# Performance work log

Hardware: AMD Instinct MI355X
Metric: run time of the kernel (lower is better)

## Reference

```python
import jax, jax.numpy as jnp
import numpy as np

N = 50000      # nodes
E = 400000     # edges (before self loops)
G = 8          # graphs in the batch
H = 128        # latent width (message_passer out_channels)
F_IN = 5       # raw node features
F_MASK = 3     # mask features (last col = BC indicator)
F_EDGE = 3     # edge_feature_dim
OUT = 3        # x-vel, y-vel, pressure
REPEATS = 3    # message passing rounds


def _mlp2(x, W1, b1, W2, b2):
    return jax.nn.relu(x @ W1 + b1) @ W2 + b2


def _seg_mean(v, ids, num):
    s = jax.ops.segment_sum(v, ids, num_segments=num)
    c = jax.ops.segment_sum(jnp.ones((v.shape[0],), v.dtype), ids, num_segments=num)
    return s / jnp.maximum(c, 1.0)[:, None]


def setup_inputs() -> dict:
    key = jax.random.key(0)
    ks = jax.random.split(key, 16)
    x = jax.random.normal(ks[0], (N, F_IN), jnp.float32)
    x_mask = (jax.random.uniform(ks[1], (N, F_MASK)) < 0.2).astype(jnp.float32)
    edge_index = jax.random.randint(ks[2], (2, E), 0, N, dtype=jnp.int32)
    edge_attr = jax.random.normal(ks[3], (E, F_EDGE), jnp.float32)
    pos = jax.random.uniform(ks[4], (N, 2), dtype=jnp.float32)
    batch = jnp.sort(jax.random.randint(ks[5], (N,), 0, G, dtype=jnp.int32))
    lin = lambda k, i, o: jax.random.normal(k, (i, o), jnp.float32) * (1.0 / np.sqrt(i))
    return {
        'x': x, 'x_mask': x_mask, 'edge_attr': edge_attr, 'pos': pos,
        'W_e1': lin(ks[6], F_IN + F_MASK, H), 'b_e1': jnp.zeros((H,), jnp.float32),
        'W_e2': lin(ks[7], H, H), 'b_e2': jnp.zeros((H,), jnp.float32),
        'W_m1': lin(ks[8], 2 * H + F_EDGE, H), 'b_m1': jnp.zeros((H,), jnp.float32),
        'W_m2': lin(ks[9], H, H), 'b_m2': jnp.zeros((H,), jnp.float32),
        'W_u1': lin(ks[10], 4 * H, H), 'b_u1': jnp.zeros((H,), jnp.float32),
        'W_u2': lin(ks[11], H, H), 'b_u2': jnp.zeros((H,), jnp.float32),
        'W_d1': lin(ks[12], H, H), 'b_d1': jnp.zeros((H,), jnp.float32),
        'W_d2': lin(ks[13], H, OUT), 'b_d2': jnp.zeros((OUT,), jnp.float32),
        'edge_index': edge_index, 'batch': batch,
    }


def reference(x, x_mask, edge_attr, pos,
              W_e1, b_e1, W_e2, b_e2,
              W_m1, b_m1, W_m2, b_m2,
              W_u1, b_u1, W_u2, b_u2,
              W_d1, b_d1, W_d2, b_d2,
              edge_index, batch):
    n = x.shape[0]
    bc = x_mask[:, -1]                                   # BC indicator (0/1)
    h = jnp.concatenate([x, x_mask], axis=1)             # [N, F_IN+F_MASK]
    # add self loops with zero edge attributes
    sl = jnp.arange(n, dtype=edge_index.dtype)
    ei = jnp.concatenate([edge_index, jnp.stack([sl, sl])], axis=1)
    ea = jnp.concatenate([edge_attr, jnp.zeros((n, edge_attr.shape[1]), edge_attr.dtype)], axis=0)
    # encoder
    h = _mlp2(h, W_e1, b_e1, W_e2, b_e2)                 # [N, H]
    # BC scatter-mean per graph and global mean pool
    bc_cnt = jax.ops.segment_sum(bc, batch, num_segments=G)
    x_BC = jax.ops.segment_sum(h * bc[:, None], batch, num_segments=G) / jnp.maximum(bc_cnt, 1.0)[:, None]
    x_graph = _seg_mean(h, batch, G)
    src, dst = ei[0], ei[1]
    for _ in range(REPEATS):
        m = _mlp2(jnp.concatenate([h[src], h[dst], ea], axis=1), W_m1, b_m1, W_m2, b_m2)
        agg = _seg_mean(m, dst, n)                       # mean aggregation at dst
        upd_in = jnp.concatenate([h, agg, x_graph[batch], x_BC[batch]], axis=1)
        h = h + _mlp2(upd_in, W_u1, b_u1, W_u2, b_u2)
        x_graph = _seg_mean(h, batch, G)
    return _mlp2(h, W_d1, b_d1, W_d2, b_d2)              # [N, OUT]
```

## Files before the change

kernel.cpp:

```cpp
#include <hip/hip_runtime.h>


#define NN 50000
#define EE 400000
#define GG 8
#define NBLK 196
#define SGRID 512

typedef __attribute__((ext_vector_type(8))) short short8;
typedef __attribute__((ext_vector_type(4))) float floatx4;

__device__ __forceinline__ unsigned short f2bf(float x) {
    unsigned u = __float_as_uint(x);
    u += 0x7FFF + ((u >> 16) & 1);
    return (unsigned short)(u >> 16);
}
__device__ __forceinline__ float bf2f(unsigned short h) {
    return __uint_as_float(((unsigned)h) << 16);
}
__device__ __forceinline__ void cvt8(const float* v, short8& hi, short8& lo) {
#pragma unroll
    for (int j = 0; j < 8; ++j) {
        unsigned short h = f2bf(v[j]);
        hi[j] = (short)h;
        lo[j] = (short)f2bf(v[j] - bf2f(h));
    }
}

__global__ void k_count(const int* __restrict__ ei, int* __restrict__ deg) {
    int i = blockIdx.x * 256 + threadIdx.x;
    if (i < EE) atomicAdd(&deg[ei[EE + i]], 1);
}

__global__ __launch_bounds__(256) void k_scan1(const int* __restrict__ deg, int* __restrict__ ex,
                                               int* __restrict__ blksum) {
    __shared__ int s[256];
    const int t = threadIdx.x;
    int i = blockIdx.x * 256 + t;
    int v = (i < NN) ? deg[i] : 0;
    s[t] = v;
    __syncthreads();
    for (int off = 1; off < 256; off <<= 1) {
        int x = (t >= off) ? s[t - off] : 0;
        __syncthreads();
        s[t] += x;
        __syncthreads();
    }
    if (i < NN) ex[i] = s[t] - v;
    if (t == 255) blksum[blockIdx.x] = s[255];
}

__global__ __launch_bounds__(256) void k_scan2(int* __restrict__ blksum) {
    __shared__ int s[256];
    const int t = threadIdx.x;
    int v = (t < NBLK) ? blksum[t] : 0;
    s[t] = v;
    __syncthreads();
    for (int off = 1; off < 256; off <<= 1) {
        int x = (t >= off) ? s[t - off] : 0;
        __syncthreads();
        s[t] += x;
        __syncthreads();
    }
    if (t < NBLK) blksum[t] = s[t] - v;
}

__global__ void k_scan3(const int* __restrict__ ex, const int* __restrict__ blkoff,
                        int* __restrict__ row_ptr, int* __restrict__ cursor) {
    int i = blockIdx.x * 256 + threadIdx.x;
    if (i < NN) {
        int v = ex[i] + blkoff[blockIdx.x];
        row_ptr[i] = v;
        cursor[i] = v;
    }
    if (i == 0) row_ptr[NN] = EE;
}

__global__ void k_scatter(const int* __restrict__ ei, const float* __restrict__ ea,
                          int* __restrict__ cursor, int* __restrict__ src_sorted,
                          float4* __restrict__ ea_s) {
    int e = blockIdx.x * 256 + threadIdx.x;
    if (e >= EE) return;
    int s = ei[e], d = ei[EE + e];
    int p = atomicAdd(&cursor[d], 1);
    src_sorted[p] = s;
    ea_s[p] = make_float4(ea[3 * e], ea[3 * e + 1], ea[3 * e + 2], 0.f);
}

__global__ __launch_bounds__(256) void k_counts(const int* __restrict__ batch, const float* __restrict__ xm,
                                                float* __restrict__ cnt_node, float* __restrict__ cnt_bc) {
    __shared__ float cn[8], cb[8];
    const int t = threadIdx.x;
    if (t < 8) { cn[t] = 0.f; cb[t] = 0.f; }
    __syncthreads();
    int i = blockIdx.x * 256 + t;
    if (i < NN) {
        int g = batch[i];
        atomicAdd(&cn[g], 1.f);
        atomicAdd(&cb[g], xm[3 * i + 2]);
    }
    __syncthreads();
    if (t < 8) {
        if (cn[t] != 0.f) atomicAdd(&cnt_node[t], cn[t]);
        if (cb[t] != 0.f) atomicAdd(&cnt_bc[t], cb[t]);
    }
}

__global__ __launch_bounds__(256) void k_wfuse(const float* __restrict__ Wm2, const float* __restrict__ Wu1,
                                               float* __restrict__ Wf) {
    int idx = blockIdx.x * 256 + threadIdx.x;
    int r = idx >> 7, c = idx & 127;
    float s = 0.f;
    for (int k = 0; k < 128; ++k) s += Wm2[r * 128 + k] * Wu1[(128 + k) * 128 + c];
    Wf[idx] = s;
}
__global__ void k_bfuse(const float* __restrict__ bm2, const float* __restrict__ Wu1,
                        const float* __restrict__ bu1, float* __restrict__ bf) {
    int c = threadIdx.x;
    float s = bu1[c];
    for (int k = 0; k < 128; ++k) s += bm2[k] * Wu1[(128 + k) * 128 + c];
    bf[c] = s;
}

__global__ __launch_bounds__(256) void k_pack_all(
    const float* __restrict__ We2, const float* __restrict__ Wm1,
    const float* __restrict__ Wu1, const float* __restrict__ Wf,
    const float* __restrict__ Wu2, const float* __restrict__ Wd1,
    short* __restrict__ We2h, short* __restrict__ We2l,
    short* __restrict__ Wm1sh, short* __restrict__ Wm1sl,
    short* __restrict__ Wm1dh, short* __restrict__ Wm1dl,
    short* __restrict__ Wu1ah, short* __restrict__ Wu1al,
    short* __restrict__ Wfh, short* __restrict__ Wfl,
    short* __restrict__ Wu2h, short* __restrict__ Wu2l,
    short* __restrict__ Wd1h, short* __restrict__ Wd1l) {
    int b = blockIdx.x;
    int id = b >> 6;
    int p = (b & 63) * 256 + threadIdx.x;
    const float* W;
    short *hi, *lo;
    switch (id) {
        case 0: W = We2; hi = We2h; lo = We2l; break;
        case 1: W = Wm1; hi = Wm1sh; lo = Wm1sl; break;
        case 2: W = Wm1 + 16384; hi = Wm1dh; lo = Wm1dl; break;
        case 3: W = Wu1; hi = Wu1ah; lo = Wu1al; break;
        case 4: W = Wf; hi = Wfh; lo = Wfl; break;
        case 5: W = Wu2; hi = Wu2h; lo = Wu2l; break;
        default: W = Wd1; hi = Wd1h; lo = Wd1l; break;
    }
    int j = p & 7;
    int lane = (p >> 3) & 63;
    int chunk = p >> 9;
    int k0 = chunk & 3, nt = chunk >> 2;
    int quad = lane >> 4;
    int n = nt * 16 + (lane & 15);
    bool perm = (id == 1) || (id == 2) || (id == 5) || (id == 6);
    int k;
    if (perm) k = k0 * 32 + ((j >> 2) << 4) + (quad << 2) + (j & 3);
    else k = k0 * 32 + quad * 8 + j;
    float w = W[k * 128 + n];
    unsigned short h = f2bf(w);
    hi[p] = (short)h;
    lo[p] = (short)f2bf(w - bf2f(h));
}

__global__ __launch_bounds__(256, 2) void k_genc(
    const float* __restrict__ x, const float* __restrict__ xm,
    const float* __restrict__ We1, const float* __restrict__ be1,
    const short* __restrict__ W2h, const short* __restrict__ W2l,
    const float* __restrict__ be2,
    const short* __restrict__ Wsh, const short* __restrict__ Wsl,
    const short* __restrict__ Wdh, const short* __restrict__ Wdl,
    const float* __restrict__ bm1, const int* __restrict__ batch,
    float* __restrict__ hout, float* __restrict__ Ps, float* __restrict__ Pd,
    float* __restrict__ part_h, float* __restrict__ part_hbc) {
    __shared__ __align__(16) short sWh[16384];
    __shared__ __align__(16) short sWl[16384];
    __shared__ __align__(16) float swe[1024];
    __shared__ float sbe[128];
    __shared__ float ldsH[1024];
    __shared__ float ldsB[1024];
    const int tid = threadIdx.x;
    const int wave = tid >> 6, lane = tid & 63;
    const int m16 = lane & 15, quad = lane >> 4;
    const int t0 = blockIdx.x * 4 + wave;
    const int t1 = t0 + SGRID * 4;
    const bool h1 = (t1 < 3125);
    const int r0 = t0 * 16 + m16;
    const int r1 = (h1 ? t1 * 16 : 0) + m16;

    auto copyW = [&](const short* gh, const short* gl) {
        const float4* sH = (const float4*)gh;
        const float4* sL = (const float4*)gl;
        float4* dH = (float4*)sWh;
        float4* dL = (float4*)sWl;
#pragma unroll
        for (int u = 0; u < 8; ++u) {
            int i = tid + u * 256;
            dH[i] = sH[i];
            dL[i] = sL[i];
        }
    };

    {
        copyW(W2h, W2l);
        for (int i = tid; i < 1024; i += 256) {
            swe[i] = We1[i];
            ldsH[i] = 0.f;
            ldsB[i] = 0.f;
        }
        if (tid < 128) sbe[tid] = be1[tid];
    }
    float in0[8], in1[8];
#pragma unroll
    for (int k = 0; k < 5; ++k) { in0[k] = x[r0 * 5 + k]; in1[k] = x[r1 * 5 + k]; }
#pragma unroll
    for (int k = 0; k < 3; ++k) { in0[5 + k] = xm[r0 * 3 + k]; in1[5 + k] = xm[r1 * 3 + k]; }
    int g0 = batch[r0], g1 = batch[r1];
    __syncthreads();
    short8 ah0[4], al0[4], ah1[4], al1[4];
#pragma unroll
    for (int k0 = 0; k0 < 4; ++k0) {
        float tv[8];
#pragma unroll
        for (int j = 0; j < 8; ++j) {
            int c = k0 * 32 + quad * 8 + j;
            float s = sbe[c];
#pragma unroll
            for (int kk = 0; kk < 8; ++kk) s += in0[kk] * swe[kk * 128 + c];
            tv[j] = fmaxf(s, 0.f);
        }
        cvt8(tv, ah0[k0], al0[k0]);
    }
#pragma unroll
    for (int k0 = 0; k0 < 4; ++k0) {
        float tv[8];
#pragma unroll
        for (int j = 0; j < 8; ++j) {
            int c = k0 * 32 + quad * 8 + j;
            float s = sbe[c];
#pragma unroll
            for (int kk = 0; kk < 8; ++kk) s += in1[kk] * swe[kk * 128 + c];
            tv[j] = fmaxf(s, 0.f);
        }
        cvt8(tv, ah1[k0], al1[k0]);
    }
    const int fb = lane << 3;
    floatx4 acc0[8], acc1[8];
    auto mmacc = [&](const short8 xh0[4], const short8 xl0[4],
                     const short8 xh1[4], const short8 xl1[4]) {
#pragma unroll
        for (int k0 = 0; k0 < 4; ++k0) {
#pragma unroll
            for (int nt = 0; nt < 8; ++nt) {
                const int base = (((nt << 2) | k0) << 9) + fb;
                short8 bh = *(const short8*)&sWh[base];
                short8 bl = *(const short8*)&sWl[base];
                acc0[nt] = __builtin_amdgcn_mfma_f32_16x16x32_bf16(bh, xh0[k0], acc0[nt], 0, 0, 0);
                acc0[nt] = __builtin_amdgcn_mfma_f32_16x16x32_bf16(bl, xh0[k0], acc0[nt], 0, 0, 0);
                acc0[nt] = __builtin_amdgcn_mfma_f32_16x16x32_bf16(bh, xl0[k0], acc0[nt], 0, 0, 0);
                if (h1) {
                    acc1[nt] = __builtin_amdgcn_mfma_f32_16x16x32_bf16(bh, xh1[k0], acc1[nt], 0, 0, 0);
                    acc1[nt] = __builtin_amdgcn_mfma_f32_16x16x32_bf16(bl, xh1[k0], acc1[nt], 0, 0, 0);
                    acc1[nt] = __builtin_amdgcn_mfma_f32_16x16x32_bf16(bh, xl1[k0], acc1[nt], 0, 0, 0);
                }
            }
        }
    };

#pragma unroll
    for (int nt = 0; nt < 8; ++nt) {
        float4 bv = *(const float4*)(be2 + nt * 16 + quad * 4);
        acc0[nt][0] = bv.x; acc0[nt][1] = bv.y; acc0[nt][2] = bv.z; acc0[nt][3] = bv.w;
        acc1[nt][0] = bv.x; acc1[nt][1] = bv.y; acc1[nt][2] = bv.z; acc1[nt][3] = bv.w;
    }
    mmacc(ah0, al0, ah1, al1);
    {
        float* d0 = hout + (size_t)r0 * 128 + quad * 4;
#pragma unroll
        for (int nt = 0; nt < 8; ++nt)
            *(float4*)(d0 + nt * 16) = make_float4(acc0[nt][0], acc0[nt][1], acc0[nt][2], acc0[nt][3]);
    }
    if (h1) {
        float* d1 = hout + (size_t)r1 * 128 + quad * 4;
#pragma unroll
        for (int nt = 0; nt < 8; ++nt)
            *(float4*)(d1 + nt * 16) = make_float4(acc1[nt][0], acc1[nt][1], acc1[nt][2], acc1[nt][3]);
    }
    {
        float bc = in0[7];
        int glo = __shfl(g0, 0), ghi = __shfl(g0, 15);
        if (glo == ghi) {
#pragma unroll
            for (int nt = 0; nt < 8; ++nt) {
                float4 v = make_float4(acc0[nt][0], acc0[nt][1], acc0[nt][2], acc0[nt][3]);
                float4 w = make_float4(v.x * bc, v.y * bc, v.z * bc, v.w * bc);
#pragma unroll
                for (int off = 1; off < 16; off <<= 1) {
                    v.x += __shfl_xor(v.x, off); v.y += __shfl_xor(v.y, off);
                    v.z += __shfl_xor(v.z, off); v.w += __shfl_xor(v.w, off);
                    w.x += __shfl_xor(w.x, off); w.y += __shfl_xor(w.y, off);
                    w.z += __shfl_xor(w.z, off); w.w += __shfl_xor(w.w, off);
                }
                if (m16 == 0) {
                    float* sp = &ldsH[glo * 128 + nt * 16 + quad * 4];
                    atomicAdd(sp + 0, v.x); atomicAdd(sp + 1, v.y);
                    atomicAdd(sp + 2, v.z); atomicAdd(sp + 3, v.w);
                    float* sq = &ldsB[glo * 128 + nt * 16 + quad * 4];
                    atomicAdd(sq + 0, w.x); atomicAdd(sq + 1, w.y);
                    atomicAdd(sq + 2, w.z); atomicAdd(sq + 3, w.w);
                }
            }
        } else {
#pragma unroll
            for (int nt = 0; nt < 8; ++nt)
#pragma unroll
                for (int i = 0; i < 4; ++i) {
                    atomicAdd(&ldsH[g0 * 128 + nt * 16 + quad * 4 + i], acc0[nt][i]);
                    atomicAdd(&ldsB[g0 * 128 + nt * 16 + quad * 4 + i], acc0[nt][i] * bc);
                }
        }
    }
    if (h1) {
        float bc = in1[7];
        int glo = __shfl(g1, 0), ghi = __shfl(g1, 15);
        if (glo == ghi) {
#pragma unroll
            for (int nt = 0; nt < 8; ++nt) {
                float4 v = make_float4(acc1[nt][0], acc1[nt][1], acc1[nt][2], acc1[nt][3]);
                float4 w = make_float4(v.x * bc, v.y * bc, v.z * bc, v.w * bc);
#pragma unroll
                for (int off = 1; off < 16; off <<= 1) {
                    v.x += __shfl_xor(v.x, off); v.y += __shfl_xor(v.y, off);
                    v.z += __shfl_xor(v.z, off); v.w += __shfl_xor(v.w, off);
                    w.x += __shfl_xor(w.x, off); w.y += __shfl_xor(w.y, off);
                    w.z += __shfl_xor(w.z, off); w.w += __shfl_xor(w.w, off);
                }
                if (m16 == 0) {
                    float* sp = &ldsH[glo * 128 + nt * 16 + quad * 4];
                    atomicAdd(sp + 0, v.x); atomicAdd(sp + 1, v.y);
                    atomicAdd(sp + 2, v.z); atomicAdd(sp + 3, v.w);
                    float* sq = &ldsB[glo * 128 + nt * 16 + quad * 4];
                    atomicAdd(sq + 0, w.x); atomicAdd(sq + 1, w.y);
                    atomicAdd(sq + 2, w.z); atomicAdd(sq + 3, w.w);
                }
            }
        } else {
#pragma unroll
            for (int nt = 0; nt < 8; ++nt)
#pragma unroll
                for (int i = 0; i < 4; ++i) {
                    atomicAdd(&ldsH[g1 * 128 + nt * 16 + quad * 4 + i], acc1[nt][i]);
                    atomicAdd(&ldsB[g1 * 128 + nt * 16 + quad * 4 + i], acc1[nt][i] * bc);
                }
        }
    }
    short8 ph0[4], pl0[4], ph1[4], pl1[4];
#pragma unroll
    for (int k0 = 0; k0 < 4; ++k0) {
        float v[8] = {acc0[2 * k0][0], acc0[2 * k0][1], acc0[2 * k0][2], acc0[2 * k0][3],
                      acc0[2 * k0 + 1][0], acc0[2 * k0 + 1][1], acc0[2 * k0 + 1][2], acc0[2 * k0 + 1][3]};
        cvt8(v, ph0[k0], pl0[k0]);
    }
#pragma unroll
    for (int k0 = 0; k0 < 4; ++k0) {
        float v[8] = {acc1[2 * k0][0], acc1[2 * k0][1], acc1[2 * k0][2], acc1[2 * k0][3],
                      acc1[2 * k0 + 1][0], acc1[2 * k0 + 1][1], acc1[2 * k0 + 1][2], acc1[2 * k0 + 1][3]};
        cvt8(v, ph1[k0], pl1[k0]);
    }
    __syncthreads();
    {
        float* ph = part_h + (size_t)blockIdx.x * 1024;
        float* pb = part_hbc + (size_t)blockIdx.x * 1024;
        for (int i = tid; i < 1024; i += 256) { ph[i] = ldsH[i]; pb[i] = ldsB[i]; }
    }
    copyW(Wsh, Wsl);
    __syncthreads();
#pragma unroll
    for (int nt = 0; nt < 8; ++nt) { acc0[nt] = (floatx4)0.f; acc1[nt] = (floatx4)0.f; }
    mmacc(ph0, pl0, ph1, pl1);
    {
        float* d0 = Ps + (size_t)r0 * 128 + quad * 4;
#pragma unroll
        for (int nt = 0; nt < 8; ++nt)
            *(float4*)(d0 + nt * 16) = make_float4(acc0[nt][0], acc0[nt][1], acc0[nt][2], acc0[nt][3]);
        if (h1) {
            float* d1 = Ps + (size_t)r1 * 128 + quad * 4;
#pragma unroll
            for (int nt = 0; nt < 8; ++nt)
                *(float4*)(d1 + nt * 16) = make_float4(acc1[nt][0], acc1[nt][1], acc1[nt][2], acc1[nt][3]);
        }
    }
    __syncthreads();
    copyW(Wdh, Wdl);
    __syncthreads();
#pragma unroll
    for (int nt = 0; nt < 8; ++nt) {
        float4 bv = *(const float4*)(bm1 + nt * 16 + quad * 4);
        acc0[nt][0] = bv.x; acc0[nt][1] = bv.y; acc0[nt][2] = bv.z; acc0[nt][3] = bv.w;
        acc1[nt][0] = bv.x; acc1[nt][1] = bv.y; acc1[nt][2] = bv.z; acc1[nt][3] = bv.w;
    }
    mmacc(ph0, pl0, ph1, pl1);
    {
        float* d0 = Pd + (size_t)r0 * 128 + quad * 4;
#pragma unroll
        for (int nt = 0; nt < 8; ++nt)
            *(float4*)(d0 + nt * 16) = make_float4(acc0[nt][0], acc0[nt][1], acc0[nt][2], acc0[nt][3]);
        if (h1) {
            float* d1 = Pd + (size_t)r1 * 128 + quad * 4;
#pragma unroll
            for (int nt = 0; nt < 8; ++nt)
                *(float4*)(d1 + nt * 16) = make_float4(acc1[nt][0], acc1[nt][1], acc1[nt][2], acc1[nt][3]);
        }
    }
}

__global__ __launch_bounds__(128) void k_redstats(const float* __restrict__ part_h,
                                                  const float* __restrict__ part_hbc,
                                                  float* __restrict__ sum_h, float* __restrict__ sum_hbc) {
    const int g = blockIdx.x, c = threadIdx.x;
    float s = 0.f, sb = 0.f;
    for (int b = 0; b < SGRID; ++b) {
        s += part_h[b * 1024 + g * 128 + c];
        sb += part_hbc[b * 1024 + g * 128 + c];
    }
    sum_h[g * 128 + c] = s;
    sum_hbc[g * 128 + c] = sb;
}

template <int MODE>
__global__ __launch_bounds__(256, 2) void k_fused3(
    const float* __restrict__ hbuf, const float* __restrict__ accm,
    const short* __restrict__ W1h, const short* __restrict__ W1l,
    const short* __restrict__ W2h, const short* __restrict__ W2l,
    const short* __restrict__ W3h, const short* __restrict__ W3l,
    const short* __restrict__ Wsh, const short* __restrict__ Wsl,
    const short* __restrict__ Wdh, const short* __restrict__ Wdl,
    const float* __restrict__ gt, const float* __restrict__ bf3,
    const float* __restrict__ bu2, const float* __restrict__ bm1,
    const float* __restrict__ bd1, const float* __restrict__ Wd2,
    const float* __restrict__ bd2, const int* __restrict__ batch,
    float* __restrict__ hout, float* __restrict__ Ps, float* __restrict__ Pd,
    float* __restrict__ partf, float* __restrict__ outp) {
    __shared__ __align__(16) short sWh[16384];
    __shared__ __align__(16) short sWl[16384];
    __shared__ float ldsH[1024];
    const int tid = threadIdx.x;
    const int wave = tid >> 6, lane = tid & 63;
    const int m16 = lane & 15, quad = lane >> 4;
    const int t0 = blockIdx.x * 4 + wave;
    const int t1 = t0 + SGRID * 4;
    const bool h1 = (t1 < 3125);
    const int r0 = t0 * 16 + m16;
    const int r1 = (h1 ? t1 * 16 : 0) + m16;

    auto copyW = [&](const short* gh, const short* gl) {
        const float4* sH = (const float4*)gh;
        const float4* sL = (const float4*)gl;
        float4* dH = (float4*)sWh;
        float4* dL = (float4*)sWl;
#pragma unroll
        for (int u = 0; u < 8; ++u) {
            int i = tid + u * 256;
            dH[i] = sH[i];
            dL[i] = sL[i];
        }
    };

    const float* Ap0 = hbuf + (size_t)r0 * 128 + quad * 8;
    const float* Ap1 = hbuf + (size_t)r1 * 128 + quad * 8;
    float4 a0[8], a1[8];
#pragma unroll
    for (int k0 = 0; k0 < 4; ++k0) {
        a0[k0 * 2 + 0] = *(const float4*)(Ap0 + k0 * 32);
        a0[k0 * 2 + 1] = *(const float4*)(Ap0 + k0 * 32 + 4);
        a1[k0 * 2 + 0] = *(const float4*)(Ap1 + k0 * 32);
        a1[k0 * 2 + 1] = *(const float4*)(Ap1 + k0 * 32 + 4);
    }
    int g0 = batch[r0], g1 = batch[r1];
    if (MODE == 0) {
        for (int i = tid; i < 1024; i += 256) ldsH[i] = 0.f;
    }
    copyW(W1h, W1l);
    __syncthreads();

    short8 hh0[4], hl0[4], hh1[4], hl1[4];
#pragma unroll
    for (int k0 = 0; k0 < 4; ++k0) {
        float v[8] = {a0[k0 * 2].x, a0[k0 * 2].y, a0[k0 * 2].z, a0[k0 * 2].w,
                      a0[k0 * 2 + 1].x, a0[k0 * 2 + 1].y, a0[k0 * 2 + 1].z, a0[k0 * 2 + 1].w};
        cvt8(v, hh0[k0], hl0[k0]);
    }
#pragma unroll
    for (int k0 = 0; k0 < 4; ++k0) {
        float v[8] = {a1[k0 * 2].x, a1[k0 * 2].y, a1[k0 * 2].z, a1[k0 * 2].w,
                      a1[k0 * 2 + 1].x, a1[k0 * 2 + 1].y, a1[k0 * 2 + 1].z, a1[k0 * 2 + 1].w};
        cvt8(v, hh1[k0], hl1[k0]);
    }

    const int fb = lane << 3;
    floatx4 acc0[8], acc1[8];
    auto mmacc = [&](const short8 xh0[4], const short8 xl0[4],
                     const short8 xh1[4], const short8 xl1[4]) {
#pragma unroll
        for (int k0 = 0; k0 < 4; ++k0) {
#pragma unroll
            for (int nt = 0; nt < 8; ++nt) {
                const int base = (((nt << 2) | k0) << 9) + fb;
                short8 bh = *(const short8*)&sWh[base];
                short8 bl = *(const short8*)&sWl[base];
                acc0[nt] = __builtin_amdgcn_mfma_f32_16x16x32_bf16(bh, xh0[k0], acc0[nt], 0, 0, 0);
                acc0[nt] = __builtin_amdgcn_mfma_f32_16x16x32_bf16(bl, xh0[k0], acc0[nt], 0, 0, 0);
                acc0[nt] = __builtin_amdgcn_mfma_f32_16x16x32_bf16(bh, xl0[k0], acc0[nt], 0, 0, 0);
                if (h1) {
                    acc1[nt] = __builtin_amdgcn_mfma_f32_16x16x32_bf16(bh, xh1[k0], acc1[nt], 0, 0, 0);
                    acc1[nt] = __builtin_amdgcn_mfma_f32_16x16x32_bf16(bl, xh1[k0], acc1[nt], 0, 0, 0);
                    acc1[nt] = __builtin_amdgcn_mfma_f32_16x16x32_bf16(bh, xl1[k0], acc1[nt], 0, 0, 0);
                }
            }
        }
    };

    {
        const float* gp0 = gt + g0 * 128 + quad * 4;
        const float* gp1 = gt + g1 * 128 + quad * 4;
#pragma unroll
        for (int nt = 0; nt < 8; ++nt) {
            float4 bv = *(const float4*)(bf3 + nt * 16 + quad * 4);
            float4 gv0 = *(const float4*)(gp0 + nt * 16);
            float4 gv1 = *(const float4*)(gp1 + nt * 16);
            acc0[nt][0] = bv.x + gv0.x; acc0[nt][1] = bv.y + gv0.y;
            acc0[nt][2] = bv.z + gv0.z; acc0[nt][3] = bv.w + gv0.w;
            acc1[nt][0] = bv.x + gv1.x; acc1[nt][1] = bv.y + gv1.y;
            acc1[nt][2] = bv.z + gv1.z; acc1[nt][3] = bv.w + gv1.w;
        }
    }
    mmacc(hh0, hl0, hh1, hl1);

    const float* Cp0 = accm + (size_t)r0 * 128 + quad * 8;
    const float* Cp1 = accm + (size_t)r1 * 128 + quad * 8;
    float4 c0[8], c1[8];
#pragma unroll
    for (int k0 = 0; k0 < 4; ++k0) {
        c0[k0 * 2 + 0] = *(const float4*)(Cp0 + k0 * 32);
        c0[k0 * 2 + 1] = *(const float4*)(Cp0 + k0 * 32 + 4);
        c1[k0 * 2 + 0] = *(const float4*)(Cp1 + k0 * 32);
        c1[k0 * 2 + 1] = *(const float4*)(Cp1 + k0 * 32 + 4);
    }
    __syncthreads();
    copyW(W2h, W2l);
    __syncthreads();

    short8 ch0[4], cl0[4], ch1[4], cl1[4];
#pragma unroll
    for (int k0 = 0; k0 < 4; ++k0) {
        float v[8] = {c0[k0 * 2].x, c0[k0 * 2].y, c0[k0 * 2].z, c0[k0 * 2].w,
                      c0[k0 * 2 + 1].x, c0[k0 * 2 + 1].y, c0[k0 * 2 + 1].z, c0[k0 * 2 + 1].w};
        cvt8(v, ch0[k0], cl0[k0]);
    }
#pragma unroll
    for (int k0 = 0; k0 < 4; ++k0) {
        float v[8] = {c1[k0 * 2].x, c1[k0 * 2].y, c1[k0 * 2].z, c1[k0 * 2].w,
                      c1[k0 * 2 + 1].x, c1[k0 * 2 + 1].y, c1[k0 * 2 + 1].z, c1[k0 * 2 + 1].w};
        cvt8(v, ch1[k0], cl1[k0]);
    }
    mmacc(ch0, cl0, ch1, cl1);

    short8 ph0[4], pl0[4], ph1[4], pl1[4];
#pragma unroll
    for (int k0 = 0; k0 < 4; ++k0) {
        float v[8] = {fmaxf(acc0[2 * k0][0], 0.f), fmaxf(acc0[2 * k0][1], 0.f),
                      fmaxf(acc0[2 * k0][2], 0.f), fmaxf(acc0[2 * k0][3], 0.f),
                      fmaxf(acc0[2 * k0 + 1][0], 0.f), fmaxf(acc0[2 * k0 + 1][1], 0.f),
                      fmaxf(acc0[2 * k0 + 1][2], 0.f), fmaxf(acc0[2 * k0 + 1][3], 0.f)};
        cvt8(v, ph0[k0], pl0[k0]);
    }
#pragma unroll
    for (int k0 = 0; k0 < 4; ++k0) {
        float v[8] = {fmaxf(acc1[2 * k0][0], 0.f), fmaxf(acc1[2 * k0][1], 0.f),
                      fmaxf(acc1[2 * k0][2], 0.f), fmaxf(acc1[2 * k0][3], 0.f),
                      fmaxf(acc1[2 * k0 + 1][0], 0.f), fmaxf(acc1[2 * k0 + 1][1], 0.f),
                      fmaxf(acc1[2 * k0 + 1][2], 0.f), fmaxf(acc1[2 * k0 + 1][3], 0.f)};
        cvt8(v, ph1[k0], pl1[k0]);
    }

    {
        const float* Ep0 = hbuf + (size_t)r0 * 128 + quad * 4;
        const float* Ep1 = hbuf + (size_t)r1 * 128 + quad * 4;
#pragma unroll
        for (int nt = 0; nt < 8; ++nt) {
            float4 bv = *(const float4*)(bu2 + nt * 16 + quad * 4);
            float4 e0 = *(const float4*)(Ep0 + nt * 16);
            float4 e1 = *(const float4*)(Ep1 + nt * 16);
            acc0[nt][0] = e0.x + bv.x; acc0[nt][1] = e0.y + bv.y;
            acc0[nt][2] = e0.z + bv.z; acc0[nt][3] = e0.w + bv.w;
            acc1[nt][0] = e1.x + bv.x; acc1[nt][1] = e1.y + bv.y;
            acc1[nt][2] = e1.z + bv.z; acc1[nt][3] = e1.w + bv.w;
        }
    }
    __syncthreads();
    copyW(W3h, W3l);
    __syncthreads();
    mmacc(ph0, pl0, ph1, pl1);

    if (MODE == 0) {
        {
            float* d0 = hout + (size_t)r0 * 128 + quad * 4;
#pragma unroll
            for (int nt = 0; nt < 8; ++nt)
                *(float4*)(d0 + nt * 16) = make_float4(acc0[nt][0], acc0[nt][1], acc0[nt][2], acc0[nt][3]);
        }
        if (h1) {
            float* d1 = hout + (size_t)r1 * 128 + quad * 4;
#pragma unroll
            for (int nt = 0; nt < 8; ++nt)
                *(float4*)(d1 + nt * 16) = make_float4(acc1[nt][0], acc1[nt][1], acc1[nt][2], acc1[nt][3]);
        }
        {
            int glo = __shfl(g0, 0), ghi = __shfl(g0, 15);
            if (glo == ghi) {
#pragma unroll
                for (int nt = 0; nt < 8; ++nt) {
                    float4 v = make_float4(acc0[nt][0], acc0[nt][1], acc0[nt][2], acc0[nt][3]);
#pragma unroll
                    for (int off = 1; off < 16; off <<= 1) {
                        v.x += __shfl_xor(v.x, off);
                        v.y += __shfl_xor(v.y, off);
                        v.z += __shfl_xor(v.z, off);
                        v.w += __shfl_xor(v.w, off);
                    }
                    if (m16 == 0) {
                        float* sp = &ldsH[glo * 128 + nt * 16 + quad * 4];
                        atomicAdd(sp + 0, v.x); atomicAdd(sp + 1, v.y);
                        atomicAdd(sp + 2, v.z); atomicAdd(sp + 3, v.w);
                    }
                }
            } else {
#pragma unroll
                for (int nt = 0; nt < 8; ++nt)
#pragma unroll
                    for (int i = 0; i < 4; ++i)
                        atomicAdd(&ldsH[g0 * 128 + nt * 16 + quad * 4 + i], acc0[nt][i]);
            }
        }
        if (h1) {
            int glo = __shfl(g1, 0), ghi = __shfl(g1, 15);
            if (glo == ghi) {
#pragma unroll
                for (int nt = 0; nt < 8; ++nt) {
                    float4 v = make_float4(acc1[nt][0], acc1[nt][1], acc1[nt][2], acc1[nt][3]);
#pragma unroll
                    for (int off = 1; off < 16; off <<= 1) {
                        v.x += __shfl_xor(v.x, off);
                        v.y += __shfl_xor(v.y, off);
                        v.z += __shfl_xor(v.z, off);
                        v.w += __shfl_xor(v.w, off);
                    }
                    if (m16 == 0) {
                        float* sp = &ldsH[glo * 128 + nt * 16 + quad * 4];
                        atomicAdd(sp + 0, v.x); atomicAdd(sp + 1, v.y);
                        atomicAdd(sp + 2, v.z); atomicAdd(sp + 3, v.w);
                    }
                }
            } else {
#pragma unroll
                for (int nt = 0; nt < 8; ++nt)
#pragma unroll
                    for (int i = 0; i < 4; ++i)
                        atomicAdd(&ldsH[g1 * 128 + nt * 16 + quad * 4 + i], acc1[nt][i]);
            }
        }
#pragma unroll
        for (int k0 = 0; k0 < 4; ++k0) {
            float v[8] = {acc0[2 * k0][0], acc0[2 * k0][1], acc0[2 * k0][2], acc0[2 * k0][3],
                          acc0[2 * k0 + 1][0], acc0[2 * k0 + 1][1], acc0[2 * k0 + 1][2], acc0[2 * k0 + 1][3]};
            cvt8(v, ph0[k0], pl0[k0]);
        }
#pragma unroll
        for (int k0 = 0; k0 < 4; ++k0) {
            float v[8] = {acc1[2 * k0][0], acc1[2 * k0][1], acc1[2 * k0][2], acc1[2 * k0][3],
                          acc1[2 * k0 + 1][0], acc1[2 * k0 + 1][1], acc1[2 * k0 + 1][2], acc1[2 * k0 + 1][3]};
            cvt8(v, ph1[k0], pl1[k0]);
        }
        __syncthreads();
        {
            float* pf = partf + (size_t)blockIdx.x * 1024;
            for (int i = tid; i < 1024; i += 256) pf[i] = ldsH[i];
        }
        copyW(Wsh, Wsl);
        __syncthreads();
#pragma unroll
        for (int nt = 0; nt < 8; ++nt) { acc0[nt] = (floatx4)0.f; acc1[nt] = (floatx4)0.f; }
        mmacc(ph0, pl0, ph1, pl1);
        {
            float* d0 = Ps + (size_t)r0 * 128 + quad * 4;
#pragma unroll
            for (int nt = 0; nt < 8; ++nt)
                *(float4*)(d0 + nt * 16) = make_float4(acc0[nt][0], acc0[nt][1], acc0[nt][2], acc0[nt][3]);
            if (h1) {
                float* d1 = Ps + (size_t)r1 * 128 + quad * 4;
#pragma unroll
                for (int nt = 0; nt < 8; ++nt)
                    *(float4*)(d1 + nt * 16) = make_float4(acc1[nt][0], acc1[nt][1], acc1[nt][2], acc1[nt][3]);
            }
        }
        __syncthreads();
        copyW(Wdh, Wdl);
        __syncthreads();
#pragma unroll
        for (int nt = 0; nt < 8; ++nt) {
            float4 bv = *(const float4*)(bm1 + nt * 16 + quad * 4);
            acc0[nt][0] = bv.x; acc0[nt][1] = bv.y; acc0[nt][2] = bv.z; acc0[nt][3] = bv.w;
            acc1[nt][0] = bv.x; acc1[nt][1] = bv.y; acc1[nt][2] = bv.z; acc1[nt][3] = bv.w;
        }
        mmacc(ph0, pl0, ph1, pl1);
        {
            float* d0 = Pd + (size_t)r0 * 128 + quad * 4;
#pragma unroll
            for (int nt = 0; nt < 8; ++nt)
                *(float4*)(d0 + nt * 16) = make_float4(acc0[nt][0], acc0[nt][1], acc0[nt][2], acc0[nt][3]);
            if (h1) {
                float* d1 = Pd + (size_t)r1 * 128 + quad * 4;
#pragma unroll
                for (int nt = 0; nt < 8; ++nt)
                    *(float4*)(d1 + nt * 16) = make_float4(acc1[nt][0], acc1[nt][1], acc1[nt][2], acc1[nt][3]);
            }
        }
    } else {
#pragma unroll
        for (int k0 = 0; k0 < 4; ++k0) {
            float v[8] = {acc0[2 * k0][0], acc0[2 * k0][1], acc0[2 * k0][2], acc0[2 * k0][3],
                          acc0[2 * k0 + 1][0], acc0[2 * k0 + 1][1], acc0[2 * k0 + 1][2], acc0[2 * k0 + 1][3]};
            cvt8(v, ph0[k0], pl0[k0]);
        }
#pragma unroll
        for (int k0 = 0; k0 < 4; ++k0) {
            float v[8] = {acc1[2 * k0][0], acc1[2 * k0][1], acc1[2 * k0][2], acc1[2 * k0][3],
                          acc1[2 * k0 + 1][0], acc1[2 * k0 + 1][1], acc1[2 * k0 + 1][2], acc1[2 * k0 + 1][3]};
            cvt8(v, ph1[k0], pl1[k0]);
        }
        __syncthreads();
        copyW(Wdh, Wdl);
        __syncthreads();
#pragma unroll
        for (int nt = 0; nt < 8; ++nt) {
            float4 bv = *(const float4*)(bd1 + nt * 16 + quad * 4);
            acc0[nt][0] = bv.x; acc0[nt][1] = bv.y; acc0[nt][2] = bv.z; acc0[nt][3] = bv.w;
            acc1[nt][0] = bv.x; acc1[nt][1] = bv.y; acc1[nt][2] = bv.z; acc1[nt][3] = bv.w;
        }
        mmacc(ph0, pl0, ph1, pl1);
        float p00 = 0.f, p01 = 0.f, p02 = 0.f, p10 = 0.f, p11 = 0.f, p12 = 0.f;
#pragma unroll
        for (int nt = 0; nt < 8; ++nt) {
#pragma unroll
            for (int i = 0; i < 4; ++i) {
                int c = nt * 16 + quad * 4 + i;
                const float* wp = &Wd2[c * 3];
                float v0 = fmaxf(acc0[nt][i], 0.f);
                float v1 = fmaxf(acc1[nt][i], 0.f);
                p00 += v0 * wp[0]; p01 += v0 * wp[1]; p02 += v0 * wp[2];
                p10 += v1 * wp[0]; p11 += v1 * wp[1]; p12 += v1 * wp[2];
            }
        }
        p00 += __shfl_xor(p00, 16); p00 += __shfl_xor(p00, 32);
        p01 += __shfl_xor(p01, 16); p01 += __shfl_xor(p01, 32);
        p02 += __shfl_xor(p02, 16); p02 += __shfl_xor(p02, 32);
        p10 += __shfl_xor(p10, 16); p10 += __shfl_xor(p10, 32);
        p11 += __shfl_xor(p11, 16); p11 += __shfl_xor(p11, 32);
        p12 += __shfl_xor(p12, 16); p12 += __shfl_xor(p12, 32);
        if (quad == 0) {
            outp[r0 * 3 + 0] = p00 + bd2[0];
            outp[r0 * 3 + 1] = p01 + bd2[1];
            outp[r0 * 3 + 2] = p02 + bd2[2];
            if (h1) {
                outp[r1 * 3 + 0] = p10 + bd2[0];
                outp[r1 * 3 + 1] = p11 + bd2[1];
                outp[r1 * 3 + 2] = p12 + bd2[2];
            }
        }
    }
}

__global__ __launch_bounds__(256) void k_edge_agg(const float* __restrict__ Ps, const float* __restrict__ Pd,
                                                  const int* __restrict__ row_ptr, const int* __restrict__ src_sorted,
                                                  const float4* __restrict__ ea_s, const float* __restrict__ Wm1,
                                                  float* __restrict__ accm) {
    const int lane = threadIdx.x & 63;
    const int d = blockIdx.x * 4 + (threadIdx.x >> 6);
    const int c = lane * 2;
    const float2 w0 = *(const float2*)&Wm1[256 * 128 + c];
    const float2 w1 = *(const float2*)&Wm1[257 * 128 + c];
    const float2 w2 = *(const float2*)&Wm1[258 * 128 + c];
    const float2 pd = *(const float2*)&Pd[(size_t)d * 128 + c];
    const int beg = row_ptr[d], end = row_ptr[d + 1];
    const float2 sv = *(const float2*)&Ps[(size_t)d * 128 + c];
    float ax = fmaxf(sv.x + pd.x, 0.f);
    float ay = fmaxf(sv.y + pd.y, 0.f);
    int k = beg;
    for (; k + 3 < end; k += 4) {
        int s0 = src_sorted[k], s1 = src_sorted[k + 1], s2 = src_sorted[k + 2], s3 = src_sorted[k + 3];
        float4 e0 = ea_s[k], e1 = ea_s[k + 1], e2 = ea_s[k + 2], e3 = ea_s[k + 3];
        float2 pa = *(const float2*)&Ps[(size_t)s0 * 128 + c];
        float2 pb = *(const float2*)&Ps[(size_t)s1 * 128 + c];
        float2 pc = *(const float2*)&Ps[(size_t)s2 * 128 + c];
        float2 pe = *(const float2*)&Ps[(size_t)s3 * 128 + c];
        ax += fmaxf(pa.x + pd.x + e0.x * w0.x + e0.y * w1.x + e0.z * w2.x, 0.f)
            + fmaxf(pb.x + pd.x + e1.x * w0.x + e1.y * w1.x + e1.z * w2.x, 0.f)
            + fmaxf(pc.x + pd.x + e2.x * w0.x + e2.y * w1.x + e2.z * w2.x, 0.f)
            + fmaxf(pe.x + pd.x + e3.x * w0.x + e3.y * w1.x + e3.z * w2.x, 0.f);
        ay += fmaxf(pa.y + pd.y + e0.x * w0.y + e0.y * w1.y + e0.z * w2.y, 0.f)
            + fmaxf(pb.y + pd.y + e1.x * w0.y + e1.y * w1.y + e1.z * w2.y, 0.f)
            + fmaxf(pc.y + pd.y + e2.x * w0.y + e2.y * w1.y + e2.z * w2.y, 0.f)
            + fmaxf(pe.y + pd.y + e3.x * w0.y + e3.y * w1.y + e3.z * w2.y, 0.f);
    }
    for (; k < end; ++k) {
        int s0 = src_sorted[k];
        float4 e0 = ea_s[k];
        float2 pa = *(const float2*)&Ps[(size_t)s0 * 128 + c];
        ax += fmaxf(pa.x + pd.x + e0.x * w0.x + e0.y * w1.x + e0.z * w2.x, 0.f);
        ay += fmaxf(pa.y + pd.y + e0.x * w0.y + e0.y * w1.y + e0.z * w2.y, 0.f);
    }
    float inv = 1.f / (float)(end - beg + 1);
    *(float2*)&accm[(size_t)d * 128 + c] = make_float2(ax * inv, ay * inv);
}

template <bool PART>
__global__ __launch_bounds__(128) void k_gterm(const float* __restrict__ sum_h, const float* __restrict__ sum_hbc,
                                               const float* __restrict__ partf,
                                               const float* __restrict__ cnt_node, const float* __restrict__ cnt_bc,
                                               const float* __restrict__ Wu1, float* __restrict__ gt) {
    const int g = blockIdx.x;
    const int c = threadIdx.x;
    __shared__ float sg[128], sb[128];
    const float invn = 1.f / fmaxf(cnt_node[g], 1.f);
    const float invb = 1.f / fmaxf(cnt_bc[g], 1.f);
    float s0;
    if (PART) {
        s0 = 0.f;
        for (int b = 0; b < SGRID; ++b) s0 += partf[b * 1024 + g * 128 + c];
    } else {
        s0 = sum_h[g * 128 + c];
    }
    sg[c] = s0 * invn;
    sb[c] = sum_hbc[g * 128 + c] * invb;
    __syncthreads();
    float s = 0.f;
    for (int k = 0; k < 128; ++k) s += sg[k] * Wu1[(256 + k) * 128 + c];
    for (int k = 0; k < 128; ++k) s += sb[k] * Wu1[(384 + k) * 128 + c];
    gt[g * 128 + c] = s;
}

extern "C" void kernel_launch(void* const* d_in, const int* in_sizes, int n_in,
                              void* d_out, int out_size, void* d_ws, size_t ws_size,
                              hipStream_t stream) {
    const float* x = (const float*)d_in[0];
    const float* x_mask = (const float*)d_in[1];
    const float* edge_attr = (const float*)d_in[2];
    const float* W_e1 = (const float*)d_in[4];
    const float* b_e1 = (const float*)d_in[5];
    const float* W_e2 = (const float*)d_in[6];
    const float* b_e2 = (const float*)d_in[7];
    const float* W_m1 = (const float*)d_in[8];
    const float* b_m1 = (const float*)d_in[9];
    const float* W_m2 = (const float*)d_in[10];
    const float* b_m2 = (const float*)d_in[11];
    const float* W_u1 = (const float*)d_in[12];
    const float* b_u1 = (const float*)d_in[13];
    const float* W_u2 = (const float*)d_in[14];
    const float* b_u2 = (const float*)d_in[15];
    const float* W_d1 = (const float*)d_in[16];
    const float* b_d1 = (const float*)d_in[17];
    const float* W_d2 = (const float*)d_in[18];
    const float* b_d2 = (const float*)d_in[19];
    const int* edge_index = (const int*)d_in[20];
    const int* batch = (const int*)d_in[21];
    float* out = (float*)d_out;

    char* wp = (char*)d_ws;
    auto carve = [&](size_t bytes) {
        char* r = wp;
        wp += (bytes + 255) & ~(size_t)255;
        return r;
    };
    float* h = (float*)carve(sizeof(float) * (size_t)NN * 128);
    float* Ps = (float*)carve(sizeof(float) * (size_t)NN * 128);
    float* Pd = (float*)carve(sizeof(float) * (size_t)NN * 128);
    float* accm = (float*)carve(sizeof(float) * (size_t)NN * 128);
    float4* ea_s = (float4*)carve(sizeof(float4) * (size_t)EE);
    float* stats = (float*)carve(sizeof(float) * 4096);
    float* sum_h = stats;
    float* sum_hbc = stats + 1024;
    float* cnt_node = stats + 2048;
    float* cnt_bc = stats + 2056;
    float* gterm = stats + 2304;
    float* bfused = stats + 3328;
    float* part_h = (float*)carve(sizeof(float) * (size_t)SGRID * 1024);
    float* part_hbc = (float*)carve(sizeof(float) * (size_t)SGRID * 1024);
    float* partf = (float*)carve(sizeof(float) * (size_t)SGRID * 1024);
    int* deg = (int*)carve(sizeof(int) * NN);
    int* row_ptr = (int*)carve(sizeof(int) * (NN + 1));
    int* cursor = (int*)carve(sizeof(int) * NN);
    int* src_sorted = (int*)carve(sizeof(int) * EE);
    int* exbuf = (int*)carve(sizeof(int) * NN);
    int* blksum = (int*)carve(sizeof(int) * 256);
    float* Wf = (float*)carve(sizeof(float) * 16384);
    short* We2h = (short*)carve(sizeof(short) * 16384);
    short* We2l = (short*)carve(sizeof(short) * 16384);
    short* Wm1sh = (short*)carve(sizeof(short) * 16384);
    short* Wm1sl = (short*)carve(sizeof(short) * 16384);
    short* Wm1dh = (short*)carve(sizeof(short) * 16384);
    short* Wm1dl = (short*)carve(sizeof(short) * 16384);
    short* Wu1ah = (short*)carve(sizeof(short) * 16384);
    short* Wu1al = (short*)carve(sizeof(short) * 16384);
    short* Wfh = (short*)carve(sizeof(short) * 16384);
    short* Wfl = (short*)carve(sizeof(short) * 16384);
    short* Wu2h = (short*)carve(sizeof(short) * 16384);
    short* Wu2l = (short*)carve(sizeof(short) * 16384);
    short* Wd1h = (short*)carve(sizeof(short) * 16384);
    short* Wd1l = (short*)carve(sizeof(short) * 16384);

    const dim3 b256(256);
    const int gE256 = (EE + 255) / 256;

    hipMemsetAsync(deg, 0, sizeof(int) * NN, stream);
    hipMemsetAsync(stats, 0, sizeof(float) * 2064, stream);
    k_wfuse<<<64, b256, 0, stream>>>(W_m2, W_u1, Wf);
    k_bfuse<<<1, 128, 0, stream>>>(b_m2, W_u1, b_u1, bfused);
    k_pack_all<<<448, b256, 0, stream>>>(W_e2, W_m1, W_u1, Wf, W_u2, W_d1,
                                         We2h, We2l, Wm1sh, Wm1sl, Wm1dh, Wm1dl,
                                         Wu1ah, Wu1al, Wfh, Wfl, Wu2h, Wu2l, Wd1h, Wd1l);
    k_count<<<gE256, b256, 0, stream>>>(edge_index, deg);
    k_scan1<<<NBLK, b256, 0, stream>>>(deg, exbuf, blksum);
    k_scan2<<<1, b256, 0, stream>>>(blksum);
    k_scan3<<<NBLK, b256, 0, stream>>>(exbuf, blksum, row_ptr, cursor);
    k_scatter<<<gE256, b256, 0, stream>>>(edge_index, edge_attr, cursor, src_sorted, ea_s);
    k_counts<<<NBLK, b256, 0, stream>>>(batch, x_mask, cnt_node, cnt_bc);
    k_genc<<<SGRID, b256, 0, stream>>>(x, x_mask, W_e1, b_e1, We2h, We2l, b_e2,
                                       Wm1sh, Wm1sl, Wm1dh, Wm1dl, b_m1, batch,
                                       h, Ps, Pd, part_h, part_hbc);
    k_redstats<<<GG, 128, 0, stream>>>(part_h, part_hbc, sum_h, sum_hbc);

    for (int rep = 0; rep < 3; ++rep) {
        if (rep == 0)
            k_gterm<false><<<GG, 128, 0, stream>>>(sum_h, sum_hbc, nullptr, cnt_node, cnt_bc, W_u1, gterm);
        else
            k_gterm<true><<<GG, 128, 0, stream>>>(nullptr, sum_hbc, partf, cnt_node, cnt_bc, W_u1, gterm);
        k_edge_agg<<<NN / 4, b256, 0, stream>>>(Ps, Pd, row_ptr, src_sorted, ea_s, W_m1, accm);
        if (rep < 2) {
            k_fused3<0><<<SGRID, b256, 0, stream>>>(h, accm, Wu1ah, Wu1al, Wfh, Wfl, Wu2h, Wu2l,
                                                    Wm1sh, Wm1sl, Wm1dh, Wm1dl,
                                                    gterm, bfused, b_u2, b_m1, nullptr, nullptr,
                                                    nullptr, batch, h, Ps, Pd, partf, nullptr);
        } else {
            k_fused3<1><<<SGRID, b256, 0, stream>>>(h, accm, Wu1ah, Wu1al, Wfh, Wfl, Wu2h, Wu2l,
                                                    nullptr, nullptr, Wd1h, Wd1l,
                                                    gterm, bfused, b_u2, nullptr, b_d1, W_d2,
                                                    b_d2, batch, nullptr, nullptr, nullptr,
                                                    nullptr, out);
        }
    }
}
```

Baseline: 626.6 us.

## Merge stats reduction and gterm into edge aggregation kernel; reuse h from registers

The separate k_redstats and k_gterm launches are removed and their work is run by extra blocks appended to the edge-aggregation grid, so the small serial reductions overlap with the edge gather. This cuts several tiny dependent launches per round. In k_fused3, the residual h values are taken from already-loaded registers via lane shuffles instead of being reloaded from global memory. That saves a global read but adds shuffle and select instructions.

```diff
diff --git a/kernel.cpp b/kernel.cpp
--- a/kernel.cpp
+++ b/kernel.cpp
@@ -187,6 +187,7 @@
     const bool h1 = (t1 < 3125);
     const int r0 = t0 * 16 + m16;
     const int r1 = (h1 ? t1 * 16 : 0) + m16;
+    (void)wave;
 
     auto copyW = [&](const short* gh, const short* gl) {
         const float4* sH = (const float4*)gh;
@@ -412,19 +413,6 @@
                 *(float4*)(d1 + nt * 16) = make_float4(acc1[nt][0], acc1[nt][1], acc1[nt][2], acc1[nt][3]);
         }
     }
-}
-
-__global__ __launch_bounds__(128) void k_redstats(const float* __restrict__ part_h,
-                                                  const float* __restrict__ part_hbc,
-                                                  float* __restrict__ sum_h, float* __restrict__ sum_hbc) {
-    const int g = blockIdx.x, c = threadIdx.x;
-    float s = 0.f, sb = 0.f;
-    for (int b = 0; b < SGRID; ++b) {
-        s += part_h[b * 1024 + g * 128 + c];
-        sb += part_hbc[b * 1024 + g * 128 + c];
-    }
-    sum_h[g * 128 + c] = s;
-    sum_hbc[g * 128 + c] = sb;
 }
 
 template <int MODE>
@@ -584,17 +572,27 @@
     }
 
     {
-        const float* Ep0 = hbuf + (size_t)r0 * 128 + quad * 4;
-        const float* Ep1 = hbuf + (size_t)r1 * 128 + quad * 4;
+        const int srcl0 = ((quad >> 1) << 4) + m16;
 #pragma unroll
         for (int nt = 0; nt < 8; ++nt) {
             float4 bv = *(const float4*)(bu2 + nt * 16 + quad * 4);
-            float4 e0 = *(const float4*)(Ep0 + nt * 16);
-            float4 e1 = *(const float4*)(Ep1 + nt * 16);
-            acc0[nt][0] = e0.x + bv.x; acc0[nt][1] = e0.y + bv.y;
-            acc0[nt][2] = e0.z + bv.z; acc0[nt][3] = e0.w + bv.w;
-            acc1[nt][0] = e1.x + bv.x; acc1[nt][1] = e1.y + bv.y;
-            acc1[nt][2] = e1.z + bv.z; acc1[nt][3] = e1.w + bv.w;
+            const int srcl = srcl0 + ((nt & 1) << 5);
+            const float4 aA0 = a0[(nt >> 1) * 2], aB0 = a0[(nt >> 1) * 2 + 1];
+            const float4 aA1 = a1[(nt >> 1) * 2], aB1 = a1[(nt >> 1) * 2 + 1];
+#pragma unroll
+            for (int i = 0; i < 4; ++i) {
+                float cA0 = (i == 0) ? aA0.x : (i == 1) ? aA0.y : (i == 2) ? aA0.z : aA0.w;
+                float cB0 = (i == 0) ? aB0.x : (i == 1) ? aB0.y : (i == 2) ? aB0.z : aB0.w;
+                float cA1 = (i == 0) ? aA1.x : (i == 1) ? aA1.y : (i == 2) ? aA1.z : aA1.w;
+                float cB1 = (i == 0) ? aB1.x : (i == 1) ? aB1.y : (i == 2) ? aB1.z : aB1.w;
+                float vA0 = __shfl(cA0, srcl), vB0 = __shfl(cB0, srcl);
+                float vA1 = __shfl(cA1, srcl), vB1 = __shfl(cB1, srcl);
+                float h0 = (quad & 1) ? vB0 : vA0;
+                float hv1 = (quad & 1) ? vB1 : vA1;
+                float b = (i == 0) ? bv.x : (i == 1) ? bv.y : (i == 2) ? bv.z : bv.w;
+                acc0[nt][i] = h0 + b;
+                acc1[nt][i] = hv1 + b;
+            }
         }
     }
     __syncthreads();
@@ -780,10 +778,48 @@
     }
 }
 
-__global__ __launch_bounds__(256) void k_edge_agg(const float* __restrict__ Ps, const float* __restrict__ Pd,
-                                                  const int* __restrict__ row_ptr, const int* __restrict__ src_sorted,
-                                                  const float4* __restrict__ ea_s, const float* __restrict__ Wm1,
-                                                  float* __restrict__ accm) {
+template <int SRC>
+__global__ __launch_bounds__(256) void k_edge_gterm(
+    const float* __restrict__ Ps, const float* __restrict__ Pd,
+    const int* __restrict__ row_ptr, const int* __restrict__ src_sorted,
+    const float4* __restrict__ ea_s, const float* __restrict__ Wm1,
+    float* __restrict__ accm,
+    const float* __restrict__ part_a, const float* __restrict__ part_b,
+    float* __restrict__ sum_hbc,
+    const float* __restrict__ cnt_node, const float* __restrict__ cnt_bc,
+    const float* __restrict__ Wu1, float* __restrict__ gt) {
+    if (blockIdx.x >= NN / 4) {
+        const int g = blockIdx.x - NN / 4;
+        const int c = threadIdx.x;
+        __shared__ float sg[128], sb[128];
+        if (c < 128) {
+            const float invn = 1.f / fmaxf(cnt_node[g], 1.f);
+            const float invb = 1.f / fmaxf(cnt_bc[g], 1.f);
+            float s0 = 0.f, sbv;
+            if (SRC == 0) {
+                float sbb = 0.f;
+                for (int b = 0; b < SGRID; ++b) {
+                    s0 += part_a[b * 1024 + g * 128 + c];
+                    sbb += part_b[b * 1024 + g * 128 + c];
+                }
+                sum_hbc[g * 128 + c] = sbb;
+                sbv = sbb;
+            } else {
+                for (int b = 0; b < SGRID; ++b) s0 += part_a[b * 1024 + g * 128 + c];
+                sbv = sum_hbc[g * 128 + c];
+            }
+            sg[c] = s0 * invn;
+            sb[c] = sbv * invb;
+        }
+        __syncthreads();
+        if (c < 128) {
+            float s = 0.f;
+            for (int k = 0; k < 128; ++k) s += sg[k] * Wu1[(256 + k) * 128 + c];
+            for (int k = 0; k < 128; ++k) s += sb[k] * Wu1[(384 + k) * 128 + c];
+            gt[g * 128 + c] = s;
+        }
+        return;
+    }
     const int lane = threadIdx.x & 63;
     const int d = blockIdx.x * 4 + (threadIdx.x >> 6);
     const int c = lane * 2;
@@ -823,32 +859,6 @@
     *(float2*)&accm[(size_t)d * 128 + c] = make_float2(ax * inv, ay * inv);
 }
 
-template <bool PART>
-__global__ __launch_bounds__(128) void k_gterm(const float* __restrict__ sum_h, const float* __restrict__ sum_hbc,
-                                               const float* __restrict__ partf,
-                                               const float* __restrict__ cnt_node, const float* __restrict__ cnt_bc,
-                                               const float* __restrict__ Wu1, float* __restrict__ gt) {
-    const int g = blockIdx.x;
-    const int c = threadIdx.x;
-    __shared__ float sg[128], sb[128];
-    const float invn = 1.f / fmaxf(cnt_node[g], 1.f);
-    const float invb = 1.f / fmaxf(cnt_bc[g], 1.f);
-    float s0;
-    if (PART) {
-        s0 = 0.f;
-        for (int b = 0; b < SGRID; ++b) s0 += partf[b * 1024 + g * 128 + c];
-    } else {
-        s0 = sum_h[g * 128 + c];
-    }
-    sg[c] = s0 * invn;
-    sb[c] = sum_hbc[g * 128 + c] * invb;
-    __syncthreads();
-    float s = 0.f;
-    for (int k = 0; k < 128; ++k) s += sg[k] * Wu1[(256 + k) * 128 + c];
-    for (int k = 0; k < 128; ++k) s += sb[k] * Wu1[(384 + k) * 128 + c];
-    gt[g * 128 + c] = s;
-}
-
 extern "C" void kernel_launch(void* const* d_in, const int* in_sizes, int n_in,
                               void* d_out, int out_size, void* d_ws, size_t ws_size,
                               hipStream_t stream) {
@@ -887,7 +897,6 @@
     float* accm = (float*)carve(sizeof(float) * (size_t)NN * 128);
     float4* ea_s = (float4*)carve(sizeof(float4) * (size_t)EE);
     float* stats = (float*)carve(sizeof(float) * 4096);
-    float* sum_h = stats;
     float* sum_hbc = stats + 1024;
     float* cnt_node = stats + 2048;
     float* cnt_bc = stats + 2056;
@@ -937,14 +946,17 @@
     k_genc<<<SGRID, b256, 0, stream>>>(x, x_mask, W_e1, b_e1, We2h, We2l, b_e2,
                                        Wm1sh, Wm1sl, Wm1dh, Wm1dl, b_m1, batch,
                                        h, Ps, Pd, part_h, part_hbc);
-    k_redstats<<<GG, 128, 0, stream>>>(part_h, part_hbc, sum_h, sum_hbc);
-
+
+    const int EGRID = NN / 4 + GG;
     for (int rep = 0; rep < 3; ++rep) {
         if (rep == 0)
-            k_gterm<false><<<GG, 128, 0, stream>>>(sum_h, sum_hbc, nullptr, cnt_node, cnt_bc, W_u1, gterm);
+            k_edge_gterm<0><<<EGRID, b256, 0, stream>>>(Ps, Pd, row_ptr, src_sorted, ea_s, W_m1, accm,
+                                                        part_h, part_hbc, sum_hbc, cnt_node, cnt_bc,
+                                                        W_u1, gterm);
         else
-            k_gterm<true><<<GG, 128, 0, stream>>>(nullptr, sum_hbc, partf, cnt_node, cnt_bc, W_u1, gterm);
-        k_edge_agg<<<NN / 4, b256, 0, stream>>>(Ps, Pd, row_ptr, src_sorted, ea_s, W_m1, accm);
+            k_edge_gterm<1><<<EGRID, b256, 0, stream>>>(Ps, Pd, row_ptr, src_sorted, ea_s, W_m1, accm,
+                                                        partf, nullptr, sum_hbc, cnt_node, cnt_bc,
+                                                        W_u1, gterm);
         if (rep < 2) {
             k_fused3<0><<<SGRID, b256, 0, stream>>>(h, accm, Wu1ah, Wu1al, Wfh, Wfl, Wu2h, Wu2l,
                                                     Wm1sh, Wm1sl, Wm1dh, Wm1dl,
```

Result: slower. 832.7 us (+32.9%).
